# Performance work log

Measured on AMD Instinct MI355X. Metric: run time of the kernel, lower is better.

## Reference

```python
import jax, jax.numpy as jnp
import numpy as np

N, E = 50000, 640000
DIN, DH, DOUT = 128, 256, 128


def _glorot(k, i, o):
    return jax.random.normal(k, (i, o), jnp.float32) / np.sqrt(i)


def setup_inputs() -> dict:
    key = jax.random.key(0)
    ks = jax.random.split(key, 12)
    return {
        "x": jax.random.normal(ks[0], (N, DIN), jnp.float32),
        "edge_index": jax.random.randint(ks[1], (2, E), 0, N, dtype=jnp.int32),
        # SAGEConv 1: in -> hidden (lin_l on aggregated w/ bias, lin_r on root)
        "W1l": _glorot(ks[2], DIN, DH), "b1l": jnp.zeros((DH,), jnp.float32), "W1r": _glorot(ks[3], DIN, DH),
        "g1": jnp.ones((DH,), jnp.float32), "be1": jnp.zeros((DH,), jnp.float32),
        # skip projection (in != hidden)
        "Wsk": _glorot(ks[4], DIN, DH), "bsk": jnp.zeros((DH,), jnp.float32),
        # SAGEConv 2: hidden -> hidden
        "W2l": _glorot(ks[5], DH, DH), "b2l": jnp.zeros((DH,), jnp.float32), "W2r": _glorot(ks[6], DH, DH),
        "g2": jnp.ones((DH,), jnp.float32), "be2": jnp.zeros((DH,), jnp.float32),
        # SAGEConv 3: hidden -> out
        "W3l": _glorot(ks[7], DH, DOUT), "b3l": jnp.zeros((DOUT,), jnp.float32), "W3r": _glorot(ks[8], DH, DOUT),
    }


def _sage_conv(x, src, dst, Wl, bl, Wr, n):
    # mean aggregation of source features into destination nodes
    msg = x[src]                                                 # [E, d]
    agg = jax.ops.segment_sum(msg, dst, num_segments=n)          # [N, d]
    cnt = jax.ops.segment_sum(jnp.ones((src.shape[0],), x.dtype), dst, num_segments=n)
    agg = agg / jnp.maximum(cnt, 1.0)[:, None]
    return agg @ Wl + bl + x @ Wr


def _layernorm(x, g, b):
    mu = jnp.mean(x, axis=-1, keepdims=True)
    var = jnp.mean((x - mu) ** 2, axis=-1, keepdims=True)
    return (x - mu) * jax.lax.rsqrt(var + 1e-5) * g + b


def reference(x, edge_index, W1l, b1l, W1r, g1, be1, Wsk, bsk,
              W2l, b2l, W2r, g2, be2, W3l, b3l, W3r):
    src, dst = edge_index[0], edge_index[1]
    n = x.shape[0]
    # layer 0: conv -> LN -> relu -> (dropout p=0, eval) -> skip via projection
    h = _sage_conv(x, src, dst, W1l, b1l, W1r, n)
    h = jax.nn.relu(_layernorm(h, g1, be1))
    h = h + (x @ Wsk + bsk)
    # layer 1: conv -> LN -> relu -> residual add (shapes match)
    h2 = _sage_conv(h, src, dst, W2l, b2l, W2r, n)
    h2 = jax.nn.relu(_layernorm(h2, g2, be2)) + h
    # final conv (no norm/act)
    return _sage_conv(h2, src, dst, W3l, b3l, W3r, n)
```

## Files before the change

kernel.cpp:

```cpp
#include <hip/hip_runtime.h>


typedef float floatx4 __attribute__((ext_vector_type(4)));
typedef short bf16x8 __attribute__((ext_vector_type(8)));

__device__ inline unsigned short f2bf(float f) {
    unsigned u = __float_as_uint(f);
    unsigned r = (u + 0x7fffu + ((u >> 16) & 1u)) >> 16;
    return (unsigned short)r;
}
__device__ inline float bf2f_lo(unsigned v) { return __uint_as_float(v << 16); }
__device__ inline float bf2f_hi(unsigned v) { return __uint_as_float(v & 0xffff0000u); }

__device__ inline void gl_lds16(const void* g, void* l) {
    __builtin_amdgcn_global_load_lds((const __attribute__((address_space(1))) unsigned int*)g,
                                     (__attribute__((address_space(3))) unsigned int*)l,
                                     16, 0, 0);
}

__global__ void hist_kernel(const int* __restrict__ dst, int* __restrict__ cnt, int E) {
    int i = blockIdx.x * blockDim.x + threadIdx.x;
    if (i < E) atomicAdd(&cnt[dst[i]], 1);
}

#define SCAN_CHUNK 2048

__global__ __launch_bounds__(256) void scan_blocksums(const int* __restrict__ cnt,
                                                      int* __restrict__ bsum, int N) {
    __shared__ int sh[256];
    int t = threadIdx.x;
    int base = blockIdx.x * SCAN_CHUNK + t * 8;
    int s = 0;
#pragma unroll
    for (int i = 0; i < 8; i++) {
        int idx = base + i;
        if (idx < N) s += cnt[idx];
    }
    sh[t] = s;
    __syncthreads();
    for (int off = 1; off < 256; off <<= 1) {
        int v = (t >= off) ? sh[t - off] : 0;
        __syncthreads();
        sh[t] += v;
        __syncthreads();
    }
    if (t == 255) bsum[blockIdx.x] = sh[255];
}

__global__ __launch_bounds__(256) void scan_bsums(const int* __restrict__ bsum,
                                                  int* __restrict__ boff, int NB,
                                                  int* __restrict__ rowptr, int N, int E) {
    __shared__ int sh[256];
    int t = threadIdx.x;
    int v = (t < NB) ? bsum[t] : 0;
    sh[t] = v;
    __syncthreads();
    for (int off = 1; off < 256; off <<= 1) {
        int u = (t >= off) ? sh[t - off] : 0;
        __syncthreads();
        sh[t] += u;
        __syncthreads();
    }
    if (t < NB) boff[t] = sh[t] - v;
    if (t == 0) rowptr[N] = E;
}

__global__ __launch_bounds__(256) void scan_final(const int* __restrict__ cnt,
                                                  const int* __restrict__ boff,
                                                  int* __restrict__ rowptr,
                                                  int* __restrict__ cursor,
                                                  float* __restrict__ invdeg, int N) {
    __shared__ int sh[256];
    int t = threadIdx.x;
    int base = blockIdx.x * SCAN_CHUNK + t * 8;
    int c[8];
    int s = 0;
#pragma unroll
    for (int i = 0; i < 8; i++) {
        int idx = base + i;
        c[i] = (idx < N) ? cnt[idx] : 0;
        s += c[i];
    }
    sh[t] = s;
    __syncthreads();
    for (int off = 1; off < 256; off <<= 1) {
        int v = (t >= off) ? sh[t - off] : 0;
        __syncthreads();
        sh[t] += v;
        __syncthreads();
    }
    int run = boff[blockIdx.x] + sh[t] - s;
#pragma unroll
    for (int i = 0; i < 8; i++) {
        int idx = base + i;
        if (idx < N) {
            rowptr[idx] = run;
            cursor[idx] = run;
            invdeg[idx] = 1.0f / (float)(c[i] > 1 ? c[i] : 1);
            run += c[i];
        }
    }
}

__global__ void scatter_kernel(const int* __restrict__ src, const int* __restrict__ dst,
                               int* __restrict__ cursor, int* __restrict__ col, int E) {
    int i = blockIdx.x * blockDim.x + threadIdx.x;
    if (i < E) {
        int p = atomicAdd(&cursor[dst[i]], 1);
        col[p] = src[i];
    }
}

__global__ void prep_weights(const float* __restrict__ W1l, const float* __restrict__ W1r,
                             const float* __restrict__ Wsk, const float* __restrict__ W2l,
                             const float* __restrict__ W2r, const float* __restrict__ W3l,
                             const float* __restrict__ W3r, const float* __restrict__ b1l,
                             const float* __restrict__ bsk,
                             unsigned short* __restrict__ WtC, unsigned short* __restrict__ Wt2,
                             unsigned short* __restrict__ Wt3, float* __restrict__ biasC) {
    int i = blockIdx.x * blockDim.x + threadIdx.x;
    if (i < 32768) {
        int k = i >> 8, n = i & 255;
        WtC[n * 256 + k] = f2bf(W1l[i]);
    } else if (i < 65536) {
        int j = i - 32768, k = j >> 8, n = j & 255;
        WtC[n * 256 + 128 + k] = f2bf(W1r[j]);
    } else if (i < 98304) {
        int j = i - 65536, k = j >> 8, n = j & 255;
        WtC[(256 + n) * 256 + 128 + k] = f2bf(Wsk[j]);
    } else if (i < 131072) {
        int j = i - 98304, k = j >> 8, n = j & 255;
        WtC[(256 + n) * 256 + k] = 0;
    } else if (i < 196608) {
        int j = i - 131072, k = j >> 8, n = j & 255;
        Wt2[n * 512 + k] = f2bf(W2l[j]);
    } else if (i < 262144) {
        int j = i - 196608, k = j >> 8, n = j & 255;
        Wt2[n * 512 + 256 + k] = f2bf(W2r[j]);
    } else if (i < 294912) {
        int j = i - 262144, k = j >> 7, n = j & 127;
        Wt3[n * 256 + k] = f2bf(W3l[j]);
    } else if (i < 327680) {
        int j = i - 294912, k = j >> 7, n = j & 127;
        Wt3[(128 + n) * 256 + k] = f2bf(W3r[j]);
    } else if (i < 328192) {
        int j = i - 327680;
        biasC[j] = (j < 256) ? b1l[j] : bsk[j - 256];
    }
}

__global__ void cvt_x_kernel(const float* __restrict__ x, unsigned short* __restrict__ A1cat, int total) {
    int i = blockIdx.x * blockDim.x + threadIdx.x;
    if (i >= total) return;
    int r = i >> 7, c = i & 127;
    A1cat[(size_t)r * 256 + 128 + c] = f2bf(x[i]);
}

__global__ __launch_bounds__(256) void agg_bf16_v2(const int* __restrict__ rowptr,
                                                   const int* __restrict__ col,
                                                   const float* __restrict__ invdeg,
                                                   const unsigned short* __restrict__ X, int xstride,
                                                   unsigned short* __restrict__ out, int ostride, int N) {
    int wid = (blockIdx.x * blockDim.x + threadIdx.x) >> 6;
    int lane = threadIdx.x & 63;
    if (wid >= N) return;
    int half = lane >> 5;
    int sub = lane & 31;
    int off = blockIdx.y * 128 + sub * 4;
    const unsigned short* Xo = X + off;
    int s = rowptr[wid], e = rowptr[wid + 1];
    float a0 = 0.f, a1 = 0.f, a2 = 0.f, a3 = 0.f;
    int j = s + half;
    for (; j + 6 < e; j += 8) {
        int c0 = col[j], c1 = col[j + 2], c2 = col[j + 4], c3 = col[j + 6];
        uint2 v0 = *(const uint2*)(Xo + (size_t)c0 * xstride);
        uint2 v1 = *(const uint2*)(Xo + (size_t)c1 * xstride);
        uint2 v2 = *(const uint2*)(Xo + (size_t)c2 * xstride);
        uint2 v3 = *(const uint2*)(Xo + (size_t)c3 * xstride);
        a0 += (bf2f_lo(v0.x) + bf2f_lo(v1.x)) + (bf2f_lo(v2.x) + bf2f_lo(v3.x));
        a1 += (bf2f_hi(v0.x) + bf2f_hi(v1.x)) + (bf2f_hi(v2.x) + bf2f_hi(v3.x));
        a2 += (bf2f_lo(v0.y) + bf2f_lo(v1.y)) + (bf2f_lo(v2.y) + bf2f_lo(v3.y));
        a3 += (bf2f_hi(v0.y) + bf2f_hi(v1.y)) + (bf2f_hi(v2.y) + bf2f_hi(v3.y));
    }
    for (; j < e; j += 2) {
        int c = col[j];
        uint2 v = *(const uint2*)(Xo + (size_t)c * xstride);
        a0 += bf2f_lo(v.x); a1 += bf2f_hi(v.x);
        a2 += bf2f_lo(v.y); a3 += bf2f_hi(v.y);
    }
    a0 += __shfl_xor(a0, 32, 64);
    a1 += __shfl_xor(a1, 32, 64);
    a2 += __shfl_xor(a2, 32, 64);
    a3 += __shfl_xor(a3, 32, 64);
    if (half == 0) {
        float inv = invdeg[wid];
        ushort4 o;
        o.x = f2bf(a0 * inv); o.y = f2bf(a1 * inv);
        o.z = f2bf(a2 * inv); o.w = f2bf(a3 * inv);
        *(ushort4*)(out + (size_t)wid * ostride + off) = o;
    }
}

__global__ __launch_bounds__(256) void agg_final_v2(const int* __restrict__ rowptr,
                                                    const int* __restrict__ col,
                                                    const float* __restrict__ invdeg,
                                                    const unsigned short* __restrict__ T,
                                                    const float* __restrict__ R,
                                                    float* __restrict__ out, int N) {
    int wid = (blockIdx.x * blockDim.x + threadIdx.x) >> 6;
    int lane = threadIdx.x & 63;
    if (wid >= N) return;
    int half = lane >> 5;
    int sub = lane & 31;
    const unsigned short* To = T + sub * 4;
    int s = rowptr[wid], e = rowptr[wid + 1];
    float a0 = 0.f, a1 = 0.f, a2 = 0.f, a3 = 0.f;
    int j = s + half;
    for (; j + 6 < e; j += 8) {
        int c0 = col[j], c1 = col[j + 2], c2 = col[j + 4], c3 = col[j + 6];
        uint2 v0 = *(const uint2*)(To + (size_t)c0 * 128);
        uint2 v1 = *(const uint2*)(To + (size_t)c1 * 128);
        uint2 v2 = *(const uint2*)(To + (size_t)c2 * 128);
        uint2 v3 = *(const uint2*)(To + (size_t)c3 * 128);
        a0 += (bf2f_lo(v0.x) + bf2f_lo(v1.x)) + (bf2f_lo(v2.x) + bf2f_lo(v3.x));
        a1 += (bf2f_hi(v0.x) + bf2f_hi(v1.x)) + (bf2f_hi(v2.x) + bf2f_hi(v3.x));
        a2 += (bf2f_lo(v0.y) + bf2f_lo(v1.y)) + (bf2f_lo(v2.y) + bf2f_lo(v3.y));
        a3 += (bf2f_hi(v0.y) + bf2f_hi(v1.y)) + (bf2f_hi(v2.y) + bf2f_hi(v3.y));
    }
    for (; j < e; j += 2) {
        int c = col[j];
        uint2 v = *(const uint2*)(To + (size_t)c * 128);
        a0 += bf2f_lo(v.x); a1 += bf2f_hi(v.x);
        a2 += bf2f_lo(v.y); a3 += bf2f_hi(v.y);
    }
    a0 += __shfl_xor(a0, 32, 64);
    a1 += __shfl_xor(a1, 32, 64);
    a2 += __shfl_xor(a2, 32, 64);
    a3 += __shfl_xor(a3, 32, 64);
    if (half == 0) {
        float inv = invdeg[wid];
        float4 r = *(const float4*)(R + (size_t)wid * 128 + sub * 4);
        float4 o;
        o.x = a0 * inv + r.x;
        o.y = a1 * inv + r.y;
        o.z = a2 * inv + r.z;
        o.w = a3 * inv + r.w;
        *(float4*)(out + (size_t)wid * 128 + sub * 4) = o;
    }
}

template <int KIT, int SPLIT>
__global__ __launch_bounds__(256) void gemm_lds(const unsigned short* __restrict__ A, int lda,
                                                const unsigned short* __restrict__ B, int ldb,
                                                const float* __restrict__ bias,
                                                unsigned short* __restrict__ C0, int ldc0,
                                                float* __restrict__ C1, int M) {
    __shared__ __align__(16) char smem[34816];
    unsigned short* sA = (unsigned short*)smem;
    unsigned short* sB = sA + 128 * 64;
    int t = threadIdx.x;
    int lane = t & 63, w = t >> 6;
    int bm = blockIdx.x * 128, bn = blockIdx.y * 128;
    int wm = (w >> 1) * 64, wn = (w & 1) * 64;
    int m16 = lane & 15, kq = lane >> 4;

    floatx4 acc[4][4];
#pragma unroll
    for (int i = 0; i < 4; i++)
#pragma unroll
        for (int j = 0; j < 4; j++) acc[i][j] = (floatx4){0.f, 0.f, 0.f, 0.f};

    const int c_row = t >> 3;
    const int kc = (t & 7) ^ (c_row & 7);
    const int srcOff = kc * 8;
    const int fsw = (m16 & 7);

    for (int kt = 0; kt < KIT; kt++) {
        int k0 = kt * 64;
#pragma unroll
        for (int i = 0; i < 4; i++) {
            int rowA = bm + i * 32 + c_row;
            if (rowA > M - 1) rowA = M - 1;
            gl_lds16(A + (size_t)rowA * lda + k0 + srcOff, (void*)&sA[(size_t)(i * 256 + t) * 8]);
            gl_lds16(B + (size_t)(bn + i * 32 + c_row) * ldb + k0 + srcOff,
                     (void*)&sB[(size_t)(i * 256 + t) * 8]);
        }
        __syncthreads();
#pragma unroll
        for (int ks = 0; ks < 2; ks++) {
            int kcl = (ks << 2) | kq;
            bf16x8 af[4], bfr[4];
#pragma unroll
            for (int mi = 0; mi < 4; mi++)
                af[mi] = *(const bf16x8*)&sA[(wm + mi * 16 + m16) * 64 + (kcl ^ fsw) * 8];
#pragma unroll
            for (int ni = 0; ni < 4; ni++)
                bfr[ni] = *(const bf16x8*)&sB[(wn + ni * 16 + m16) * 64 + (kcl ^ fsw) * 8];
#pragma unroll
            for (int mi = 0; mi < 4; mi++)
#pragma unroll
                for (int ni = 0; ni < 4; ni++)
                    acc[mi][ni] = __builtin_amdgcn_mfma_f32_16x16x32_bf16(af[mi], bfr[ni], acc[mi][ni], 0, 0, 0);
        }
        __syncthreads();
    }

    float* wb = (float*)smem + w * (64 * 34);
    const float* bias0 = (SPLIT == 0) ? bias : ((bn == 0) ? nullptr : bias);
#pragma unroll
    for (int h = 0; h < 2; h++) {
#pragma unroll
        for (int nj = 0; nj < 2; nj++) {
            int ni = h * 2 + nj;
#pragma unroll
            for (int mi = 0; mi < 4; mi++)
#pragma unroll
                for (int r = 0; r < 4; r++)
                    wb[(mi * 16 + kq * 4 + r) * 34 + nj * 16 + m16] = acc[mi][ni][r];
        }
        asm volatile("s_waitcnt lgkmcnt(0)" ::: "memory");
        if (SPLIT == 0 || bn == 0) {
            int rsub = lane >> 2, c8 = (lane & 3) * 8;
            int ldc = (SPLIT == 0) ? ldc0 : 128;
            int gcol = ((SPLIT == 0) ? bn : 0) + wn + h * 32 + c8;
            float bv[8];
#pragma unroll
            for (int j = 0; j < 8; j++) bv[j] = bias0 ? bias0[gcol + j] : 0.f;
#pragma unroll
            for (int it = 0; it < 4; it++) {
                int rr = it * 16 + rsub;
                int grow = bm + wm + rr;
                float v0 = wb[rr * 34 + c8 + 0] + bv[0];
                float v1 = wb[rr * 34 + c8 + 1] + bv[1];
                float v2 = wb[rr * 34 + c8 + 2] + bv[2];
                float v3 = wb[rr * 34 + c8 + 3] + bv[3];
                float v4 = wb[rr * 34 + c8 + 4] + bv[4];
                float v5 = wb[rr * 34 + c8 + 5] + bv[5];
                float v6 = wb[rr * 34 + c8 + 6] + bv[6];
                float v7 = wb[rr * 34 + c8 + 7] + bv[7];
                uint4 o;
                o.x = (unsigned)f2bf(v0) | ((unsigned)f2bf(v1) << 16);
                o.y = (unsigned)f2bf(v2) | ((unsigned)f2bf(v3) << 16);
                o.z = (unsigned)f2bf(v4) | ((unsigned)f2bf(v5) << 16);
                o.w = (unsigned)f2bf(v6) | ((unsigned)f2bf(v7) << 16);
                if (grow < M) *(uint4*)(C0 + (size_t)grow * ldc + gcol) = o;
            }
        } else {
            int rsub = lane >> 3, c4 = (lane & 7) * 4;
            int gcol = wn + h * 32 + c4;
            float bv[4];
#pragma unroll
            for (int j = 0; j < 4; j++) bv[j] = bias0[gcol + j];
#pragma unroll
            for (int it = 0; it < 8; it++) {
                int rr = it * 8 + rsub;
                int grow = bm + wm + rr;
                float4 o;
                o.x = wb[rr * 34 + c4 + 0] + bv[0];
                o.y = wb[rr * 34 + c4 + 1] + bv[1];
                o.z = wb[rr * 34 + c4 + 2] + bv[2];
                o.w = wb[rr * 34 + c4 + 3] + bv[3];
                if (grow < M) *(float4*)(C1 + (size_t)grow * 128 + gcol) = o;
            }
        }
        if (h == 0) asm volatile("s_waitcnt lgkmcnt(0)" ::: "memory");
    }
}

__global__ __launch_bounds__(256) void ln_fuse2(const unsigned short* __restrict__ u, int ustride,
                                                const unsigned short* __restrict__ a, int astride,
                                                const float* __restrict__ g, const float* __restrict__ b,
                                                unsigned short* __restrict__ out, int ostride, int N) {
    int row = (blockIdx.x * blockDim.x + threadIdx.x) >> 6;
    int lane = threadIdx.x & 63;
    if (row >= N) return;
    uint2 uv = *(const uint2*)(u + (size_t)row * ustride + lane * 4);
    float v0 = bf2f_lo(uv.x), v1 = bf2f_hi(uv.x), v2 = bf2f_lo(uv.y), v3 = bf2f_hi(uv.y);
    float s = (v0 + v1) + (v2 + v3);
    float sq = (v0 * v0 + v1 * v1) + (v2 * v2 + v3 * v3);
    for (int off = 1; off < 64; off <<= 1) {
        s += __shfl_xor(s, off, 64);
        sq += __shfl_xor(sq, off, 64);
    }
    float mu = s * (1.f / 256.f);
    float var = sq * (1.f / 256.f) - mu * mu;
    float rs = rsqrtf(var + 1e-5f);
    float4 gv = *(const float4*)(g + lane * 4);
    float4 bv = *(const float4*)(b + lane * 4);
    uint2 av = *(const uint2*)(a + (size_t)row * astride + lane * 4);
    float a0 = bf2f_lo(av.x), a1 = bf2f_hi(av.x), a2 = bf2f_lo(av.y), a3 = bf2f_hi(av.y);
    ushort4 o;
    o.x = f2bf(fmaxf((v0 - mu) * rs * gv.x + bv.x, 0.f) + a0);
    o.y = f2bf(fmaxf((v1 - mu) * rs * gv.y + bv.y, 0.f) + a1);
    o.z = f2bf(fmaxf((v2 - mu) * rs * gv.z + bv.z, 0.f) + a2);
    o.w = f2bf(fmaxf((v3 - mu) * rs * gv.w + bv.w, 0.f) + a3);
    *(ushort4*)(out + (size_t)row * ostride + lane * 4) = o;
}

extern "C" void kernel_launch(void* const* d_in, const int* in_sizes, int n_in,
                              void* d_out, int out_size, void* d_ws, size_t ws_size,
                              hipStream_t stream) {
    const float* x   = (const float*)d_in[0];
    const int*   ei  = (const int*)d_in[1];
    const float* W1l = (const float*)d_in[2];
    const float* b1l = (const float*)d_in[3];
    const float* W1r = (const float*)d_in[4];
    const float* g1  = (const float*)d_in[5];
    const float* be1 = (const float*)d_in[6];
    const float* Wsk = (const float*)d_in[7];
    const float* bsk = (const float*)d_in[8];
    const float* W2l = (const float*)d_in[9];
    const float* b2l = (const float*)d_in[10];
    const float* W2r = (const float*)d_in[11];
    const float* g2  = (const float*)d_in[12];
    const float* be2 = (const float*)d_in[13];
    const float* W3l = (const float*)d_in[14];
    const float* b3l = (const float*)d_in[15];
    const float* W3r = (const float*)d_in[16];

    const int N = in_sizes[0] / 128;
    const int E = in_sizes[1] / 2;
    const int* src = ei;
    const int* dst = ei + E;

    char* p = (char*)d_ws;
    auto alloc = [&](size_t bytes) {
        void* r = (void*)p;
        p += (bytes + 255) & ~(size_t)255;
        return r;
    };
    int*   cnt    = (int*)alloc(sizeof(int) * N);
    int*   rowptr = (int*)alloc(sizeof(int) * (N + 1));
    int*   cursor = (int*)alloc(sizeof(int) * N);
    float* invdeg = (float*)alloc(sizeof(float) * N);
    int*   col    = (int*)alloc(sizeof(int) * E);
    int*   bsum   = (int*)alloc(sizeof(int) * 256);
    int*   boff   = (int*)alloc(sizeof(int) * 256);
    unsigned short* A1cat = (unsigned short*)alloc(sizeof(short) * (size_t)N * 256);
    unsigned short* A2cat = (unsigned short*)alloc(sizeof(short) * (size_t)N * 512);
    unsigned short* U1    = (unsigned short*)alloc(sizeof(short) * (size_t)N * 512);
    float* r3 = (float*)alloc(sizeof(float) * (size_t)N * 128);
    unsigned short* WtC = (unsigned short*)alloc(sizeof(short) * 512 * 256);
    unsigned short* Wt2 = (unsigned short*)alloc(sizeof(short) * 256 * 512);
    unsigned short* Wt3 = (unsigned short*)alloc(sizeof(short) * 256 * 256);
    float* biasC = (float*)alloc(sizeof(float) * 512);
    unsigned short* t3 = A1cat;
    unsigned short* u2 = U1;

    hipMemsetAsync(cnt, 0, sizeof(int) * N, stream);
    hist_kernel<<<(E + 255) / 256, 256, 0, stream>>>(dst, cnt, E);
    int NB = (N + SCAN_CHUNK - 1) / SCAN_CHUNK;
    scan_blocksums<<<NB, 256, 0, stream>>>(cnt, bsum, N);
    scan_bsums<<<1, 256, 0, stream>>>(bsum, boff, NB, rowptr, N, E);
    scan_final<<<NB, 256, 0, stream>>>(cnt, boff, rowptr, cursor, invdeg, N);
    scatter_kernel<<<(E + 255) / 256, 256, 0, stream>>>(src, dst, cursor, col, E);

    prep_weights<<<(328192 + 255) / 256, 256, 0, stream>>>(W1l, W1r, Wsk, W2l, W2r, W3l, W3r,
                                                           b1l, bsk, WtC, Wt2, Wt3, biasC);
    cvt_x_kernel<<<((N * 128) + 255) / 256, 256, 0, stream>>>(x, A1cat, N * 128);

    int aggBlocks = (N + 3) / 4;
    int mBlocks = (N + 127) / 128;

    agg_bf16_v2<<<dim3(aggBlocks, 1), 256, 0, stream>>>(rowptr, col, invdeg, A1cat + 128, 256, A1cat, 256, N);
    gemm_lds<4, 0><<<dim3(mBlocks, 4), 256, 0, stream>>>(A1cat, 256, WtC, 256, biasC, U1, 512, nullptr, N);
    ln_fuse2<<<aggBlocks, 256, 0, stream>>>(U1, 512, U1 + 256, 512, g1, be1, A2cat + 256, 512, N);

    agg_bf16_v2<<<dim3(aggBlocks, 2), 256, 0, stream>>>(rowptr, col, invdeg, A2cat + 256, 512, A2cat, 512, N);
    gemm_lds<8, 0><<<dim3(mBlocks, 2), 256, 0, stream>>>(A2cat, 512, Wt2, 512, b2l, u2, 256, nullptr, N);
    ln_fuse2<<<aggBlocks, 256, 0, stream>>>(u2, 256, A2cat + 256, 512, g2, be2, A2cat, 512, N);

    gemm_lds<4, 1><<<dim3(mBlocks, 2), 256, 0, stream>>>(A2cat, 512, Wt3, 256, b3l, t3, 128, r3, N);
    agg_final_v2<<<aggBlocks, 256, 0, stream>>>(rowptr, col, invdeg, t3, r3, (float*)d_out, N);
}
```

Measured before the change: 420.8 us.

## Gather layer-2 neighbor features in FP8 and mask tail edges in aggregation loops

The first layer-norm kernel also writes an FP8 copy of its output. The layer-2 aggregation then gathers these 256-wide FP8 rows in one pass, halving the bytes read per neighbour compared with the bf16 gather. Separately, all aggregation loops drop the scalar tail loop and instead clamp indices and multiply by 0/1 masks, so every iteration issues four independent loads. The cost is reduced precision in the layer-2 mean aggregation, plus an extra FP8 buffer write in the layer-norm kernel.

After: 410.4 us. 2.5% less time.

```diff
diff --git a/kernel.cpp b/kernel.cpp
--- a/kernel.cpp
+++ b/kernel.cpp
@@ -2,7 +2,17 @@
 
 
 typedef float floatx4 __attribute__((ext_vector_type(4)));
+typedef float floatx2 __attribute__((ext_vector_type(2)));
 typedef short bf16x8 __attribute__((ext_vector_type(8)));
+
+#if defined(__has_builtin)
+#if __has_builtin(__builtin_amdgcn_cvt_pk_f32_fp8) && __has_builtin(__builtin_amdgcn_cvt_pk_fp8_f32)
+#define HAS_FP8_CVT 1
+#endif
+#endif
+#ifndef HAS_FP8_CVT
+#define HAS_FP8_CVT 0
+#endif
 
 __device__ inline unsigned short f2bf(float f) {
     unsigned u = __float_as_uint(f);
@@ -156,7 +166,7 @@
     A1cat[(size_t)r * 256 + 128 + c] = f2bf(x[i]);
 }
 
-__global__ __launch_bounds__(256) void agg_bf16_v2(const int* __restrict__ rowptr,
+__global__ __launch_bounds__(256) void agg_bf16_v3(const int* __restrict__ rowptr,
                                                    const int* __restrict__ col,
                                                    const float* __restrict__ invdeg,
                                                    const unsigned short* __restrict__ X, int xstride,
@@ -170,23 +180,25 @@
     const unsigned short* Xo = X + off;
     int s = rowptr[wid], e = rowptr[wid + 1];
     float a0 = 0.f, a1 = 0.f, a2 = 0.f, a3 = 0.f;
-    int j = s + half;
-    for (; j + 6 < e; j += 8) {
-        int c0 = col[j], c1 = col[j + 2], c2 = col[j + 4], c3 = col[j + 6];
+    for (int j = s + half; j < e; j += 8) {
+        int j1 = (j + 2 < e) ? j + 2 : j;
+        int j2 = (j + 4 < e) ? j + 4 : j;
+        int j3 = (j + 6 < e) ? j + 6 : j;
+        float m1 = (j + 2 < e) ? 1.f : 0.f;
+        float m2 = (j + 4 < e) ? 1.f : 0.f;
+        float m3 = (j + 6 < e) ? 1.f : 0.f;
+        int c0 = col[j], c1 = col[j1], c2 = col[j2], c3 = col[j3];
         uint2 v0 = *(const uint2*)(Xo + (size_t)c0 * xstride);
         uint2 v1 = *(const uint2*)(Xo + (size_t)c1 * xstride);
         uint2 v2 = *(const uint2*)(Xo + (size_t)c2 * xstride);
         uint2 v3 = *(const uint2*)(Xo + (size_t)c3 * xstride);
-        a0 += (bf2f_lo(v0.x) + bf2f_lo(v1.x)) + (bf2f_lo(v2.x) + bf2f_lo(v3.x));
-        a1 += (bf2f_hi(v0.x) + bf2f_hi(v1.x)) + (bf2f_hi(v2.x) + bf2f_hi(v3.x));
-        a2 += (bf2f_lo(v0.y) + bf2f_lo(v1.y)) + (bf2f_lo(v2.y) + bf2f_lo(v3.y));
-        a3 += (bf2f_hi(v0.y) + bf2f_hi(v1.y)) + (bf2f_hi(v2.y) + bf2f_hi(v3.y));
-    }
-    for (; j < e; j += 2) {
-        int c = col[j];
-        uint2 v = *(const uint2*)(Xo + (size_t)c * xstride);
-        a0 += bf2f_lo(v.x); a1 += bf2f_hi(v.x);
-        a2 += bf2f_lo(v.y); a3 += bf2f_hi(v.y);
+        a0 += bf2f_lo(v0.x); a1 += bf2f_hi(v0.x); a2 += bf2f_lo(v0.y); a3 += bf2f_hi(v0.y);
+        a0 = fmaf(m1, bf2f_lo(v1.x), a0); a1 = fmaf(m1, bf2f_hi(v1.x), a1);
+        a2 = fmaf(m1, bf2f_lo(v1.y), a2); a3 = fmaf(m1, bf2f_hi(v1.y), a3);
+        a0 = fmaf(m2, bf2f_lo(v2.x), a0); a1 = fmaf(m2, bf2f_hi(v2.x), a1);
+        a2 = fmaf(m2, bf2f_lo(v2.y), a2); a3 = fmaf(m2, bf2f_hi(v2.y), a3);
+        a0 = fmaf(m3, bf2f_lo(v3.x), a0); a1 = fmaf(m3, bf2f_hi(v3.x), a1);
+        a2 = fmaf(m3, bf2f_lo(v3.y), a2); a3 = fmaf(m3, bf2f_hi(v3.y), a3);
     }
     a0 += __shfl_xor(a0, 32, 64);
     a1 += __shfl_xor(a1, 32, 64);
@@ -201,7 +213,60 @@
     }
 }
 
-__global__ __launch_bounds__(256) void agg_final_v2(const int* __restrict__ rowptr,
+#if HAS_FP8_CVT
+__device__ inline void accum_fp8(uint2 v, float m, float* a) {
+    floatx2 p;
+    p = __builtin_amdgcn_cvt_pk_f32_fp8(v.x, false); a[0] = fmaf(m, p.x, a[0]); a[1] = fmaf(m, p.y, a[1]);
+    p = __builtin_amdgcn_cvt_pk_f32_fp8(v.x, true);  a[2] = fmaf(m, p.x, a[2]); a[3] = fmaf(m, p.y, a[3]);
+    p = __builtin_amdgcn_cvt_pk_f32_fp8(v.y, false); a[4] = fmaf(m, p.x, a[4]); a[5] = fmaf(m, p.y, a[5]);
+    p = __builtin_amdgcn_cvt_pk_f32_fp8(v.y, true);  a[6] = fmaf(m, p.x, a[6]); a[7] = fmaf(m, p.y, a[7]);
+}
+
+__global__ __launch_bounds__(256) void agg_fp8_256(const int* __restrict__ rowptr,
+                                                   const int* __restrict__ col,
+                                                   const float* __restrict__ invdeg,
+                                                   const unsigned char* __restrict__ H8,
+                                                   unsigned short* __restrict__ out, int ostride, int N) {
+    int wid = (blockIdx.x * blockDim.x + threadIdx.x) >> 6;
+    int lane = threadIdx.x & 63;
+    if (wid >= N) return;
+    int half = lane >> 5;
+    int sub = lane & 31;
+    const unsigned char* Ho = H8 + sub * 8;
+    int s = rowptr[wid], e = rowptr[wid + 1];
+    float a[8] = {0.f, 0.f, 0.f, 0.f, 0.f, 0.f, 0.f, 0.f};
+    for (int j = s + half; j < e; j += 8) {
+        int j1 = (j + 2 < e) ? j + 2 : j;
+        int j2 = (j + 4 < e) ? j + 4 : j;
+        int j3 = (j + 6 < e) ? j + 6 : j;
+        float m1 = (j + 2 < e) ? 1.f : 0.f;
+        float m2 = (j + 4 < e) ? 1.f : 0.f;
+        float m3 = (j + 6 < e) ? 1.f : 0.f;
+        int c0 = col[j], c1 = col[j1], c2 = col[j2], c3 = col[j3];
+        uint2 v0 = *(const uint2*)(Ho + (size_t)c0 * 256);
+        uint2 v1 = *(const uint2*)(Ho + (size_t)c1 * 256);
+        uint2 v2 = *(const uint2*)(Ho + (size_t)c2 * 256);
+        uint2 v3 = *(const uint2*)(Ho + (size_t)c3 * 256);
+        accum_fp8(v0, 1.f, a);
+        accum_fp8(v1, m1, a);
+        accum_fp8(v2, m2, a);
+        accum_fp8(v3, m3, a);
+    }
+#pragma unroll
+    for (int i = 0; i < 8; i++) a[i] += __shfl_xor(a[i], 32, 64);
+    if (half == 0) {
+        float inv = invdeg[wid];
+        uint4 o;
+        o.x = (unsigned)f2bf(a[0] * inv) | ((unsigned)f2bf(a[1] * inv) << 16);
+        o.y = (unsigned)f2bf(a[2] * inv) | ((unsigned)f2bf(a[3] * inv) << 16);
+        o.z = (unsigned)f2bf(a[4] * inv) | ((unsigned)f2bf(a[5] * inv) << 16);
+        o.w = (unsigned)f2bf(a[6] * inv) | ((unsigned)f2bf(a[7] * inv) << 16);
+        *(uint4*)(out + (size_t)wid * ostride + sub * 8) = o;
+    }
+}
+#endif
+
+__global__ __launch_bounds__(256) void agg_final_v3(const int* __restrict__ rowptr,
                                                     const int* __restrict__ col,
                                                     const float* __restrict__ invdeg,
                                                     const unsigned short* __restrict__ T,
@@ -215,23 +280,25 @@
     const unsigned short* To = T + sub * 4;
     int s = rowptr[wid], e = rowptr[wid + 1];
     float a0 = 0.f, a1 = 0.f, a2 = 0.f, a3 = 0.f;
-    int j = s + half;
-    for (; j + 6 < e; j += 8) {
-        int c0 = col[j], c1 = col[j + 2], c2 = col[j + 4], c3 = col[j + 6];
+    for (int j = s + half; j < e; j += 8) {
+        int j1 = (j + 2 < e) ? j + 2 : j;
+        int j2 = (j + 4 < e) ? j + 4 : j;
+        int j3 = (j + 6 < e) ? j + 6 : j;
+        float m1 = (j + 2 < e) ? 1.f : 0.f;
+        float m2 = (j + 4 < e) ? 1.f : 0.f;
+        float m3 = (j + 6 < e) ? 1.f : 0.f;
+        int c0 = col[j], c1 = col[j1], c2 = col[j2], c3 = col[j3];
         uint2 v0 = *(const uint2*)(To + (size_t)c0 * 128);
         uint2 v1 = *(const uint2*)(To + (size_t)c1 * 128);
         uint2 v2 = *(const uint2*)(To + (size_t)c2 * 128);
         uint2 v3 = *(const uint2*)(To + (size_t)c3 * 128);
-        a0 += (bf2f_lo(v0.x) + bf2f_lo(v1.x)) + (bf2f_lo(v2.x) + bf2f_lo(v3.x));
-        a1 += (bf2f_hi(v0.x) + bf2f_hi(v1.x)) + (bf2f_hi(v2.x) + bf2f_hi(v3.x));
-        a2 += (bf2f_lo(v0.y) + bf2f_lo(v1.y)) + (bf2f_lo(v2.y) + bf2f_lo(v3.y));
-        a3 += (bf2f_hi(v0.y) + bf2f_hi(v1.y)) + (bf2f_hi(v2.y) + bf2f_hi(v3.y));
-    }
-    for (; j < e; j += 2) {
-        int c = col[j];
-        uint2 v = *(const uint2*)(To + (size_t)c * 128);
-        a0 += bf2f_lo(v.x); a1 += bf2f_hi(v.x);
-        a2 += bf2f_lo(v.y); a3 += bf2f_hi(v.y);
+        a0 += bf2f_lo(v0.x); a1 += bf2f_hi(v0.x); a2 += bf2f_lo(v0.y); a3 += bf2f_hi(v0.y);
+        a0 = fmaf(m1, bf2f_lo(v1.x), a0); a1 = fmaf(m1, bf2f_hi(v1.x), a1);
+        a2 = fmaf(m1, bf2f_lo(v1.y), a2); a3 = fmaf(m1, bf2f_hi(v1.y), a3);
+        a0 = fmaf(m2, bf2f_lo(v2.x), a0); a1 = fmaf(m2, bf2f_hi(v2.x), a1);
+        a2 = fmaf(m2, bf2f_lo(v2.y), a2); a3 = fmaf(m2, bf2f_hi(v2.y), a3);
+        a0 = fmaf(m3, bf2f_lo(v3.x), a0); a1 = fmaf(m3, bf2f_hi(v3.x), a1);
+        a2 = fmaf(m3, bf2f_lo(v3.y), a2); a3 = fmaf(m3, bf2f_hi(v3.y), a3);
     }
     a0 += __shfl_xor(a0, 32, 64);
     a1 += __shfl_xor(a1, 32, 64);
@@ -370,7 +437,8 @@
 __global__ __launch_bounds__(256) void ln_fuse2(const unsigned short* __restrict__ u, int ustride,
                                                 const unsigned short* __restrict__ a, int astride,
                                                 const float* __restrict__ g, const float* __restrict__ b,
-                                                unsigned short* __restrict__ out, int ostride, int N) {
+                                                unsigned short* __restrict__ out, int ostride,
+                                                unsigned char* __restrict__ h8, int N) {
     int row = (blockIdx.x * blockDim.x + threadIdx.x) >> 6;
     int lane = threadIdx.x & 63;
     if (row >= N) return;
@@ -389,12 +457,21 @@
     float4 bv = *(const float4*)(b + lane * 4);
     uint2 av = *(const uint2*)(a + (size_t)row * astride + lane * 4);
     float a0 = bf2f_lo(av.x), a1 = bf2f_hi(av.x), a2 = bf2f_lo(av.y), a3 = bf2f_hi(av.y);
+    float o0 = fmaxf((v0 - mu) * rs * gv.x + bv.x, 0.f) + a0;
+    float o1 = fmaxf((v1 - mu) * rs * gv.y + bv.y, 0.f) + a1;
+    float o2 = fmaxf((v2 - mu) * rs * gv.z + bv.z, 0.f) + a2;
+    float o3 = fmaxf((v3 - mu) * rs * gv.w + bv.w, 0.f) + a3;
     ushort4 o;
-    o.x = f2bf(fmaxf((v0 - mu) * rs * gv.x + bv.x, 0.f) + a0);
-    o.y = f2bf(fmaxf((v1 - mu) * rs * gv.y + bv.y, 0.f) + a1);
-    o.z = f2bf(fmaxf((v2 - mu) * rs * gv.z + bv.z, 0.f) + a2);
-    o.w = f2bf(fmaxf((v3 - mu) * rs * gv.w + bv.w, 0.f) + a3);
+    o.x = f2bf(o0); o.y = f2bf(o1); o.z = f2bf(o2); o.w = f2bf(o3);
     *(ushort4*)(out + (size_t)row * ostride + lane * 4) = o;
+#if HAS_FP8_CVT
+    if (h8) {
+        unsigned wpk = 0;
+        wpk = __builtin_amdgcn_cvt_pk_fp8_f32(o0, o1, wpk, false);
+        wpk = __builtin_amdgcn_cvt_pk_fp8_f32(o2, o3, wpk, true);
+        *(unsigned*)(h8 + (size_t)row * 256 + lane * 4) = wpk;
+    }
+#endif
 }
 
 extern "C" void kernel_launch(void* const* d_in, const int* in_sizes, int n_in,
@@ -440,6 +517,7 @@
     unsigned short* A2cat = (unsigned short*)alloc(sizeof(short) * (size_t)N * 512);
     unsigned short* U1    = (unsigned short*)alloc(sizeof(short) * (size_t)N * 512);
     float* r3 = (float*)alloc(sizeof(float) * (size_t)N * 128);
+    unsigned char* H8 = (unsigned char*)alloc((size_t)N * 256);
     unsigned short* WtC = (unsigned short*)alloc(sizeof(short) * 512 * 256);
     unsigned short* Wt2 = (unsigned short*)alloc(sizeof(short) * 256 * 512);
     unsigned short* Wt3 = (unsigned short*)alloc(sizeof(short) * 256 * 256);
@@ -462,14 +540,18 @@
     int aggBlocks = (N + 3) / 4;
     int mBlocks = (N + 127) / 128;
 
-    agg_bf16_v2<<<dim3(aggBlocks, 1), 256, 0, stream>>>(rowptr, col, invdeg, A1cat + 128, 256, A1cat, 256, N);
+    agg_bf16_v3<<<dim3(aggBlocks, 1), 256, 0, stream>>>(rowptr, col, invdeg, A1cat + 128, 256, A1cat, 256, N);
     gemm_lds<4, 0><<<dim3(mBlocks, 4), 256, 0, stream>>>(A1cat, 256, WtC, 256, biasC, U1, 512, nullptr, N);
-    ln_fuse2<<<aggBlocks, 256, 0, stream>>>(U1, 512, U1 + 256, 512, g1, be1, A2cat + 256, 512, N);
-
-    agg_bf16_v2<<<dim3(aggBlocks, 2), 256, 0, stream>>>(rowptr, col, invdeg, A2cat + 256, 512, A2cat, 512, N);
+    ln_fuse2<<<aggBlocks, 256, 0, stream>>>(U1, 512, U1 + 256, 512, g1, be1, A2cat + 256, 512, H8, N);
+
+#if HAS_FP8_CVT
+    agg_fp8_256<<<aggBlocks, 256, 0, stream>>>(rowptr, col, invdeg, H8, A2cat, 512, N);
+#else
+    agg_bf16_v3<<<dim3(aggBlocks, 2), 256, 0, stream>>>(rowptr, col, invdeg, A2cat + 256, 512, A2cat, 512, N);
+#endif
     gemm_lds<8, 0><<<dim3(mBlocks, 2), 256, 0, stream>>>(A2cat, 512, Wt2, 512, b2l, u2, 256, nullptr, N);
-    ln_fuse2<<<aggBlocks, 256, 0, stream>>>(u2, 256, A2cat + 256, 512, g2, be2, A2cat, 512, N);
+    ln_fuse2<<<aggBlocks, 256, 0, stream>>>(u2, 256, A2cat + 256, 512, g2, be2, A2cat, 512, nullptr, N);
 
     gemm_lds<4, 1><<<dim3(mBlocks, 2), 256, 0, stream>>>(A2cat, 512, Wt3, 256, b3l, t3, 128, r3, N);
-    agg_final_v2<<<aggBlocks, 256, 0, stream>>>(rowptr, col, invdeg, t3, r3, (float*)d_out, N);
-}
+    agg_final_v3<<<aggBlocks, 256, 0, stream>>>(rowptr, col, invdeg, t3, r3, (float*)d_out, N);
+}
```
